# Kernel tuning notes

Measured on AMD Instinct MI355X. Metric: run time of the kernel, lower is better.

The kernel has to match this reference:

```python
import jax, jax.numpy as jnp
import numpy as np

D_MODEL = 2048
HEADDIM = 32
NHEADS = D_MODEL // HEADDIM  # 64
BLOCK = 256
EPS = 1e-4


def segsum(x):
    # x: (..., T) -> (..., T, T) stable segment sums, -inf above diagonal
    T = x.shape[-1]
    xe = jnp.broadcast_to(x[..., None], x.shape + (T,))  # (..., d, e)
    lower = jnp.tril(jnp.ones((T, T), dtype=bool), -1)
    xe = jnp.where(lower, xe, 0.0)
    s = jnp.cumsum(xe, axis=-2)
    incl = jnp.tril(jnp.ones((T, T), dtype=bool), 0)
    return jnp.where(incl, s, -jnp.inf)


def ssd_minimal_discrete(X, A, B, C, block_len):
    # X: (b, L, h, p); A: (b, L, h); B, C: (b, L, h, n). L % block_len == 0.
    b, Lm, h, p = X.shape
    c = Lm // block_len
    Xb = X.reshape(b, c, block_len, h, p)
    Bb = B.reshape(b, c, block_len, h, B.shape[-1])
    Cb = C.reshape(b, c, block_len, h, C.shape[-1])
    Ab = A.reshape(b, c, block_len, h).transpose(0, 3, 1, 2)  # (b, h, c, l)
    A_cumsum = jnp.cumsum(Ab, axis=-1)
    Lmat = jnp.exp(segsum(Ab))  # (b, h, c, l, s)
    # 1. intra-chunk (diagonal block) output
    Y_diag = jnp.einsum('bclhn,bcshn,bhcls,bcshp->bclhp', Cb, Bb, Lmat, Xb)
    # 2. per-chunk states
    decay_states = jnp.exp(A_cumsum[:, :, :, -1:] - A_cumsum)  # (b, h, c, l)
    states = jnp.einsum('bclhn,bhcl,bclhp->bchpn', Bb, decay_states, Xb)
    # 3. inter-chunk recurrence
    init = jnp.zeros_like(states[:, :1])
    states = jnp.concatenate([init, states], axis=1)  # (b, c+1, h, p, n)
    A_last = jnp.pad(A_cumsum[:, :, :, -1], ((0, 0), (0, 0), (1, 0)))  # (b, h, c+1)
    decay_chunk = jnp.exp(segsum(A_last))  # (b, h, c+1, c+1)
    new_states = jnp.einsum('bhzc,bchpn->bzhpn', decay_chunk, states)
    states_in, final_state = new_states[:, :-1], new_states[:, -1]
    # 4. state -> output within chunks
    state_decay_out = jnp.exp(A_cumsum)  # (b, h, c, l)
    Y_off = jnp.einsum('bclhn,bchpn,bhcl->bclhp', Cb, states_in, state_decay_out)
    Y = (Y_diag + Y_off).reshape(b, Lm, h, p)
    return Y, final_state


def setup_inputs() -> dict:
    key = jax.random.key(0)
    k1, k2 = jax.random.split(key)
    Bsz, Lfull, M = 2, 4096, 2048
    hidden_states = jax.random.normal(k1, (Bsz, M, D_MODEL), dtype=jnp.float32)
    # boundaries at even positions: exactly M boundaries per row, position 0 is a boundary
    boundary_mask = jnp.broadcast_to((jnp.arange(Lfull) % 2 == 0)[None, :], (Bsz, Lfull))
    boundary_prob = jax.random.uniform(k2, (Bsz, Lfull, 2), dtype=jnp.float32)
    mask = jnp.ones((Bsz, Lfull), dtype=bool)
    return {"hidden_states": hidden_states, "boundary_mask": boundary_mask,
            "boundary_prob": boundary_prob, "mask": mask}


def reference(hidden_states, boundary_mask, boundary_prob, mask):
    Bsz, Lfull = boundary_mask.shape
    M = hidden_states.shape[1]
    # select boundary-position probabilities, in order, first M
    p = jnp.clip(boundary_prob[..., -1].astype(jnp.float32), EPS, 1.0 - EPS)
    token_idx = jnp.arange(Lfull)[None, :] + (~boundary_mask).astype(jnp.int32) * Lfull
    order = jnp.argsort(token_idx, axis=1, stable=True)
    p_sel = jnp.take_along_axis(p, order[:, :M], axis=1)  # (B, M)
    dt = jnp.log(1.0 / (1.0 - p_sel))
    x = hidden_states.astype(jnp.float32) / dt[..., None]
    Xr = x.reshape(Bsz, M, NHEADS, HEADDIM)
    A_dt = -jnp.broadcast_to(dt[:, :, None], (Bsz, M, NHEADS))  # A = -1, A*dt
    B_ssd = jnp.broadcast_to(p_sel[:, :, None, None], (Bsz, M, NHEADS, 1))
    C_ssd = jnp.ones_like(B_ssd)
    out, _ = ssd_minimal_discrete(Xr, A_dt, B_ssd, C_ssd, BLOCK)
    out = out.reshape(Bsz, M, D_MODEL)
    # plug back: each uncompressed token reads the EMA value of its chunk
    plug = jnp.cumsum(boundary_mask.astype(jnp.int32), axis=1) - 1  # (B, L)
    out = jnp.take_along_axis(out, plug[:, :, None], axis=1)  # (B, L, d_model)
    return out
```

## Files before the change

### kernel.cpp

```cpp
#include <hip/hip_runtime.h>
#include <math.h>

#define BSZ    2
#define LFULL  4096
#define MLEN   2048
#define DMODEL 2048
#define CLIP_EPS 1e-4f
#define CCH    256
#define TCH    8

typedef float f4 __attribute__((ext_vector_type(4)));

__global__ __launch_bounds__(1024, 2) void mega(
    const float* __restrict__ hid, const int* __restrict__ bmask_raw,
    const float* __restrict__ bprob, float* __restrict__ out)
{
  const int tid = threadIdx.x;
  const int j   = tid & 3;
  const int c   = tid >> 2;
  const int bx  = blockIdx.x;
  const int b   = blockIdx.y;

  __shared__ union {
    struct { int cnt[257]; int mode; int ntrue; int sel[MLEN]; } k1;
    struct { float P[CCH]; f4 S[CCH][4]; } scan;
  } sm;

  const int d4 = bx * 4 + j;
  const int o  = b * MLEN + c * TCH;
  const f4* xp = (const f4*)hid + ((size_t)o * DMODEL >> 2) + d4;
  f4 xr[TCH];
  #pragma unroll
  for (int t = 0; t < TCH; ++t) xr[t] = xp[(size_t)t * (DMODEL / 4)];

  if (tid == 0) {
    unsigned w0 = ((const unsigned*)bmask_raw)[0];
    sm.k1.mode = (w0 <= 1u) ? 1 : 0;
  }
  __syncthreads();
  const int mode = sm.k1.mode;
  const unsigned char* bmask_u8 = (const unsigned char*)bmask_raw;

  const int PER = LFULL / 256;
  if (tid < 256) {
    const int base = tid * PER;
    int cnt = 0;
    for (int i = 0; i < PER; ++i) {
      const int L = base + i;
      const int v = mode ? (bmask_raw[b * LFULL + L] != 0)
                         : (bmask_u8[b * LFULL + L] != 0);
      cnt += v;
    }
    sm.k1.cnt[tid] = cnt;
  }
  __syncthreads();

  if (tid < 64) {
    const int q = tid * 4;
    const int c0 = sm.k1.cnt[q], c1 = sm.k1.cnt[q + 1];
    const int c2 = sm.k1.cnt[q + 2], c3 = sm.k1.cnt[q + 3];
    const int mysum = c0 + c1 + c2 + c3;
    int incl = mysum;
    #pragma unroll
    for (int off = 1; off < 64; off <<= 1) {
      const int v = __shfl_up(incl, off, 64);
      if (tid >= off) incl += v;
    }
    const int excl = incl - mysum;
    sm.k1.cnt[q]     = excl;
    sm.k1.cnt[q + 1] = excl + c0;
    sm.k1.cnt[q + 2] = excl + c0 + c1;
    sm.k1.cnt[q + 3] = excl + c0 + c1 + c2;
    if (tid == 63) { sm.k1.cnt[256] = incl; sm.k1.ntrue = incl; }
  }
  __syncthreads();
  const int ntrue = sm.k1.ntrue;

  if (tid < 256) {
    const int base = tid * PER;
    int trun = sm.k1.cnt[tid];
    for (int i = 0; i < PER; ++i) {
      const int L = base + i;
      const int v = mode ? (bmask_raw[b * LFULL + L] != 0)
                         : (bmask_u8[b * LFULL + L] != 0);
      if (v) {
        if (trun < MLEN) sm.k1.sel[trun] = L;
        ++trun;
      } else {
        const int f = L - trun;
        const int slot = ntrue + f;
        if (slot < MLEN) sm.k1.sel[slot] = L;
      }
    }
  }
  __syncthreads();

  const int nb = (ntrue < MLEN) ? ntrue : MLEN;
  float w[TCH], e[TCH], cd[TCH];
  int   ls[TCH], le[TCH];
  {
    float run = 1.0f;
    #pragma unroll
    for (int t = 0; t < TCH; ++t) {
      const int g = c * TCH + t;
      const int L = sm.k1.sel[g];
      float p = bprob[((size_t)b * LFULL + L) * 2 + 1];
      p = fminf(fmaxf(p, CLIP_EPS), 1.0f - CLIP_EPS);
      const float dt = -log1pf(-p);
      w[t] = p / dt;
      e[t] = 1.0f - p;
      run *= e[t];
      cd[t] = run;
      if (nb == 0) {
        ls[t] = (g == 0) ? 0 : LFULL;
        le[t] = (g == 0) ? LFULL : LFULL;
      } else if (g < nb) {
        ls[t] = (g == 0) ? 0 : sm.k1.sel[g];
        le[t] = (g == nb - 1) ? LFULL : sm.k1.sel[g + 1];
      } else {
        ls[t] = LFULL; le[t] = LFULL;
      }
    }
  }
  __syncthreads();

  f4 st = {0.f, 0.f, 0.f, 0.f};
  #pragma unroll
  for (int t = 0; t < TCH; ++t) {
    const f4 x = xr[t];
    st.x = fmaf(e[t], st.x, w[t] * x.x);
    st.y = fmaf(e[t], st.y, w[t] * x.y);
    st.z = fmaf(e[t], st.z, w[t] * x.z);
    st.w = fmaf(e[t], st.w, w[t] * x.w);
    xr[t] = st;
  }
  sm.scan.S[c][j] = st;
  if (j == 0) sm.scan.P[c] = cd[TCH - 1];
  __syncthreads();

  for (int dstep = 1; dstep < CCH; dstep <<= 1) {
    const float pc = sm.scan.P[c];
    float pd = 1.0f;
    f4 sd = {0.f, 0.f, 0.f, 0.f};
    if (c >= dstep) { pd = sm.scan.P[c - dstep]; sd = sm.scan.S[c - dstep][j]; }
    __syncthreads();
    if (c >= dstep) {
      f4 cur = sm.scan.S[c][j];
      cur.x = fmaf(pc, sd.x, cur.x);
      cur.y = fmaf(pc, sd.y, cur.y);
      cur.z = fmaf(pc, sd.z, cur.z);
      cur.w = fmaf(pc, sd.w, cur.w);
      sm.scan.S[c][j] = cur;
      if (j == 0) sm.scan.P[c] = pc * pd;
    }
    __syncthreads();
  }

  f4 H = {0.f, 0.f, 0.f, 0.f};
  if (c > 0) H = sm.scan.S[c - 1][j];

  f4* op = (f4*)out + ((size_t)b * LFULL * DMODEL >> 2) + d4;
  #pragma unroll
  for (int t = 0; t < TCH; ++t) {
    f4 y;
    y.x = fmaf(cd[t], H.x, xr[t].x);
    y.y = fmaf(cd[t], H.y, xr[t].y);
    y.z = fmaf(cd[t], H.z, xr[t].z);
    y.w = fmaf(cd[t], H.w, xr[t].w);
    for (int L = ls[t]; L < le[t]; ++L) {
      __builtin_nontemporal_store(y, op + (size_t)L * (DMODEL / 4));
    }
  }
}

extern "C" void kernel_launch(void* const* d_in, const int* in_sizes, int n_in,
                              void* d_out, int out_size, void* d_ws, size_t ws_size,
                              hipStream_t stream) {
  const float* hid   = (const float*)d_in[0];
  const int*   bmask = (const int*)d_in[1];
  const float* bprob = (const float*)d_in[2];
  float*       out   = (float*)d_out;
  (void)d_ws; (void)ws_size;

  mega<<<dim3(DMODEL / 16, BSZ), dim3(1024), 0, stream>>>(hid, bmask, bprob, out);
}
```

Measured before the change: 119.0 us.

## Spread boundary scan over all threads and drop shared-memory union

The boundary-mask count and compaction now run on all 1024 threads (4 entries each) instead of 256, using a two-level wave-shuffle prefix scan in place of the single-wave scan. The shared-memory union is split into separate arrays so the selection indices stay valid through the output phase, and the per-token ls/le ranges are computed there rather than held in registers, which also removes one barrier. An empty asm constraint forces the prefetched hidden-state loads to be issued early. Shared memory per block grows, which may affect the two-blocks-per-CU occupancy target.

```diff
diff --git a/kernel.cpp b/kernel.cpp
--- a/kernel.cpp
+++ b/kernel.cpp
@@ -21,10 +21,11 @@
   const int bx  = blockIdx.x;
   const int b   = blockIdx.y;
 
-  __shared__ union {
-    struct { int cnt[257]; int mode; int ntrue; int sel[MLEN]; } k1;
-    struct { float P[CCH]; f4 S[CCH][4]; } scan;
-  } sm;
+  __shared__ int   s_sel[MLEN];
+  __shared__ float s_P[CCH];
+  __shared__ f4    s_S[CCH][4];
+  __shared__ int   s_wtot[16];
+  __shared__ int   s_mode, s_ntrue;
 
   const int d4 = bx * 4 + j;
   const int o  = b * MLEN + c * TCH;
@@ -32,78 +33,75 @@
   f4 xr[TCH];
   #pragma unroll
   for (int t = 0; t < TCH; ++t) xr[t] = xp[(size_t)t * (DMODEL / 4)];
+  #pragma unroll
+  for (int t = 0; t < TCH; ++t) asm volatile("" : "+v"(xr[t]));
 
   if (tid == 0) {
     unsigned w0 = ((const unsigned*)bmask_raw)[0];
-    sm.k1.mode = (w0 <= 1u) ? 1 : 0;
+    s_mode = (w0 <= 1u) ? 1 : 0;
   }
   __syncthreads();
-  const int mode = sm.k1.mode;
+  const int mode = s_mode;
   const unsigned char* bmask_u8 = (const unsigned char*)bmask_raw;
 
-  const int PER = LFULL / 256;
-  if (tid < 256) {
-    const int base = tid * PER;
-    int cnt = 0;
+  const int PER  = LFULL / 1024;
+  const int base = tid * PER;
+
+  int cnt = 0;
+  {
+    #pragma unroll
     for (int i = 0; i < PER; ++i) {
       const int L = base + i;
       const int v = mode ? (bmask_raw[b * LFULL + L] != 0)
                          : (bmask_u8[b * LFULL + L] != 0);
       cnt += v;
     }
-    sm.k1.cnt[tid] = cnt;
+  }
+
+  const int lane = tid & 63, wv = tid >> 6;
+  int incl = cnt;
+  #pragma unroll
+  for (int off = 1; off < 64; off <<= 1) {
+    const int v = __shfl_up(incl, off, 64);
+    if (lane >= off) incl += v;
+  }
+  if (lane == 63) s_wtot[wv] = incl;
+  __syncthreads();
+  if (tid == 0) {
+    int run = 0;
+    #pragma unroll
+    for (int w = 0; w < 16; ++w) { const int t = s_wtot[w]; s_wtot[w] = run; run += t; }
+    s_ntrue = run;
   }
   __syncthreads();
+  const int excl  = (incl - cnt) + s_wtot[wv];
+  const int ntrue = s_ntrue;
 
-  if (tid < 64) {
-    const int q = tid * 4;
-    const int c0 = sm.k1.cnt[q], c1 = sm.k1.cnt[q + 1];
-    const int c2 = sm.k1.cnt[q + 2], c3 = sm.k1.cnt[q + 3];
-    const int mysum = c0 + c1 + c2 + c3;
-    int incl = mysum;
+  {
+    int trun = excl;
     #pragma unroll
-    for (int off = 1; off < 64; off <<= 1) {
-      const int v = __shfl_up(incl, off, 64);
-      if (tid >= off) incl += v;
-    }
-    const int excl = incl - mysum;
-    sm.k1.cnt[q]     = excl;
-    sm.k1.cnt[q + 1] = excl + c0;
-    sm.k1.cnt[q + 2] = excl + c0 + c1;
-    sm.k1.cnt[q + 3] = excl + c0 + c1 + c2;
-    if (tid == 63) { sm.k1.cnt[256] = incl; sm.k1.ntrue = incl; }
-  }
-  __syncthreads();
-  const int ntrue = sm.k1.ntrue;
-
-  if (tid < 256) {
-    const int base = tid * PER;
-    int trun = sm.k1.cnt[tid];
     for (int i = 0; i < PER; ++i) {
       const int L = base + i;
       const int v = mode ? (bmask_raw[b * LFULL + L] != 0)
                          : (bmask_u8[b * LFULL + L] != 0);
       if (v) {
-        if (trun < MLEN) sm.k1.sel[trun] = L;
+        if (trun < MLEN) s_sel[trun] = L;
         ++trun;
       } else {
         const int f = L - trun;
         const int slot = ntrue + f;
-        if (slot < MLEN) sm.k1.sel[slot] = L;
+        if (slot < MLEN) s_sel[slot] = L;
       }
     }
   }
   __syncthreads();
 
-  const int nb = (ntrue < MLEN) ? ntrue : MLEN;
   float w[TCH], e[TCH], cd[TCH];
-  int   ls[TCH], le[TCH];
   {
     float run = 1.0f;
     #pragma unroll
     for (int t = 0; t < TCH; ++t) {
-      const int g = c * TCH + t;
-      const int L = sm.k1.sel[g];
+      const int L = s_sel[c * TCH + t];
       float p = bprob[((size_t)b * LFULL + L) * 2 + 1];
       p = fminf(fmaxf(p, CLIP_EPS), 1.0f - CLIP_EPS);
       const float dt = -log1pf(-p);
@@ -111,18 +109,8 @@
       e[t] = 1.0f - p;
       run *= e[t];
       cd[t] = run;
-      if (nb == 0) {
-        ls[t] = (g == 0) ? 0 : LFULL;
-        le[t] = (g == 0) ? LFULL : LFULL;
-      } else if (g < nb) {
-        ls[t] = (g == 0) ? 0 : sm.k1.sel[g];
-        le[t] = (g == nb - 1) ? LFULL : sm.k1.sel[g + 1];
-      } else {
-        ls[t] = LFULL; le[t] = LFULL;
-      }
     }
   }
-  __syncthreads();
 
   f4 st = {0.f, 0.f, 0.f, 0.f};
   #pragma unroll
@@ -134,40 +122,52 @@
     st.w = fmaf(e[t], st.w, w[t] * x.w);
     xr[t] = st;
   }
-  sm.scan.S[c][j] = st;
-  if (j == 0) sm.scan.P[c] = cd[TCH - 1];
+  s_S[c][j] = st;
+  if (j == 0) s_P[c] = cd[TCH - 1];
   __syncthreads();
 
   for (int dstep = 1; dstep < CCH; dstep <<= 1) {
-    const float pc = sm.scan.P[c];
+    const float pc = s_P[c];
     float pd = 1.0f;
     f4 sd = {0.f, 0.f, 0.f, 0.f};
-    if (c >= dstep) { pd = sm.scan.P[c - dstep]; sd = sm.scan.S[c - dstep][j]; }
+    if (c >= dstep) { pd = s_P[c - dstep]; sd = s_S[c - dstep][j]; }
     __syncthreads();
     if (c >= dstep) {
-      f4 cur = sm.scan.S[c][j];
+      f4 cur = s_S[c][j];
       cur.x = fmaf(pc, sd.x, cur.x);
       cur.y = fmaf(pc, sd.y, cur.y);
       cur.z = fmaf(pc, sd.z, cur.z);
       cur.w = fmaf(pc, sd.w, cur.w);
-      sm.scan.S[c][j] = cur;
-      if (j == 0) sm.scan.P[c] = pc * pd;
+      s_S[c][j] = cur;
+      if (j == 0) s_P[c] = pc * pd;
     }
     __syncthreads();
   }
 
   f4 H = {0.f, 0.f, 0.f, 0.f};
-  if (c > 0) H = sm.scan.S[c - 1][j];
+  if (c > 0) H = s_S[c - 1][j];
 
+  const int nb = (ntrue < MLEN) ? ntrue : MLEN;
   f4* op = (f4*)out + ((size_t)b * LFULL * DMODEL >> 2) + d4;
   #pragma unroll
   for (int t = 0; t < TCH; ++t) {
+    const int g = c * TCH + t;
+    int ls, le;
+    if (nb == 0) {
+      ls = (g == 0) ? 0 : LFULL;
+      le = (g == 0) ? LFULL : LFULL;
+    } else if (g < nb) {
+      ls = (g == 0) ? 0 : s_sel[g];
+      le = (g == nb - 1) ? LFULL : s_sel[g + 1];
+    } else {
+      ls = LFULL; le = LFULL;
+    }
     f4 y;
     y.x = fmaf(cd[t], H.x, xr[t].x);
     y.y = fmaf(cd[t], H.y, xr[t].y);
     y.z = fmaf(cd[t], H.z, xr[t].z);
     y.w = fmaf(cd[t], H.w, xr[t].w);
-    for (int L = ls[t]; L < le[t]; ++L) {
+    for (int L = ls; L < le; ++L) {
       __builtin_nontemporal_store(y, op + (size_t)L * (DMODEL / 4));
     }
   }
```

Result: faster. 116.6 us (-2.0%).
